# Performance work log

Measured on AMD Instinct MI355X. Metric: run time of the kernel, lower is better.

Reference implementation:

```python
import jax, jax.numpy as jnp
import numpy as np

NUM_HEADS = 8
QUERY_HEAD_DIM = 32
POS_HEAD_DIM = 4
EMBED_DIM = 512
POS_DIM = 192
SEQ_LEN = 1024
BATCH = 8
IN_PROJ_DIM = (QUERY_HEAD_DIM * 2 + POS_HEAD_DIM) * NUM_HEADS  # 544


def setup_inputs() -> dict:
    key = jax.random.key(0)
    k1, k2, k3, k4, k5 = jax.random.split(key, 5)
    x = jax.random.normal(k1, (SEQ_LEN, BATCH, EMBED_DIM), dtype=jnp.float32)
    pos_emb = jax.random.normal(k2, (1, 2 * SEQ_LEN - 1, POS_DIM), dtype=jnp.float32)
    key_padding_mask = jnp.zeros((BATCH, SEQ_LEN), dtype=bool)
    # in_proj: ScaledLinear(embed_dim -> in_proj_dim) with initial_scale qhd**-0.25
    scale_in = QUERY_HEAD_DIM ** (-0.25) / np.sqrt(EMBED_DIM)
    W_in = jax.random.normal(k3, (EMBED_DIM, IN_PROJ_DIM), dtype=jnp.float32) * scale_in
    b_in = jax.random.normal(k4, (IN_PROJ_DIM,), dtype=jnp.float32) * 0.01
    # linear_pos: ScaledLinear(pos_dim -> num_heads*pos_head_dim), no bias, scale 0.05
    W_pos = jax.random.normal(k5, (POS_DIM, NUM_HEADS * POS_HEAD_DIM), dtype=jnp.float32) * (0.05 / np.sqrt(POS_DIM))
    return {"x": x, "pos_emb": pos_emb, "W_in": W_in, "b_in": b_in,
            "W_pos": W_pos, "key_padding_mask": key_padding_mask}


def reference(x, pos_emb, W_in, b_in, W_pos, key_padding_mask):
    S, B, _ = x.shape
    H, QH, PH = NUM_HEADS, QUERY_HEAD_DIM, POS_HEAD_DIM
    qd = H * QH
    xp = x @ W_in + b_in                          # (S, B, in_proj_dim)
    q = xp[..., :qd].reshape(S, B, H, QH)
    k = xp[..., qd:2 * qd].reshape(S, B, H, QH)   # Whiten/Balancer are identity in eval
    p = xp[..., 2 * qd:].reshape(S, B, H, PH)
    # content scores: (H, B, T, Sk)
    attn_scores = jnp.einsum('tbhd,sbhd->hbts', q, k)
    # positional scores
    pe = (pos_emb @ W_pos).reshape(2 * S - 1, H, PH)          # (2S-1, H, PH)
    pos_scores = jnp.einsum('tbhd,nhd->hbtn', p, pe)          # (H, B, T, 2S-1)
    # relative shift: out[h,b,t,j] = pos_scores[h,b,t, (S-1) - t + j]
    idx = (S - 1) - jnp.arange(S)[:, None] + jnp.arange(S)[None, :]  # (S, S)
    shifted = jnp.take_along_axis(pos_scores, idx[None, None, :, :], axis=-1)
    attn_scores = attn_scores + shifted
    # key padding mask: True positions get -1000 (as in masked_fill)
    attn_scores = jnp.where(key_padding_mask[None, :, None, :], -1000.0, attn_scores)
    return jax.nn.softmax(attn_scores, axis=-1)  # (H, B, T, S)
```

## Files before the change

kernel.cpp:

```cpp
#include <hip/hip_runtime.h>

#define SEQ  1024
#define BATCH 8
#define NH   8
#define EMB  512
#define QHD  32
#define PHD  4
#define PDIM 192
#define NPROJ 544
#define NPE  2047
#define L2E  1.4426950408889634f

typedef float nf4 __attribute__((ext_vector_type(4)));
typedef short bf16x8 __attribute__((ext_vector_type(8)));
typedef float f32x4 __attribute__((ext_vector_type(4)));

__device__ __forceinline__ unsigned short f2bf_rne(float f) {
    unsigned int u = __float_as_uint(f);
    unsigned int r = (u + 0x7fffu + ((u >> 16) & 1u)) >> 16;
    return (unsigned short)r;
}
__device__ __forceinline__ float bf2f(unsigned short b) {
    return __uint_as_float(((unsigned int)b) << 16);
}
__device__ __forceinline__ void cvt8(const float4 a, const float4 b, uint4& hi, uint4& lo) {
    unsigned short h0 = f2bf_rne(a.x), h1 = f2bf_rne(a.y), h2 = f2bf_rne(a.z), h3 = f2bf_rne(a.w);
    unsigned short h4 = f2bf_rne(b.x), h5 = f2bf_rne(b.y), h6 = f2bf_rne(b.z), h7 = f2bf_rne(b.w);
    unsigned short l0 = f2bf_rne(a.x - bf2f(h0)), l1 = f2bf_rne(a.y - bf2f(h1));
    unsigned short l2 = f2bf_rne(a.z - bf2f(h2)), l3 = f2bf_rne(a.w - bf2f(h3));
    unsigned short l4 = f2bf_rne(b.x - bf2f(h4)), l5 = f2bf_rne(b.y - bf2f(h5));
    unsigned short l6 = f2bf_rne(b.z - bf2f(h6)), l7 = f2bf_rne(b.w - bf2f(h7));
    hi.x = (unsigned)h0 | ((unsigned)h1 << 16); hi.y = (unsigned)h2 | ((unsigned)h3 << 16);
    hi.z = (unsigned)h4 | ((unsigned)h5 << 16); hi.w = (unsigned)h6 | ((unsigned)h7 << 16);
    lo.x = (unsigned)l0 | ((unsigned)l1 << 16); lo.y = (unsigned)l2 | ((unsigned)l3 << 16);
    lo.z = (unsigned)l4 | ((unsigned)l5 << 16); lo.w = (unsigned)l6 | ((unsigned)l7 << 16);
}

__global__ __launch_bounds__(256) void convw_kernel(const float* __restrict__ W,
                                                    unsigned short* __restrict__ whT,
                                                    unsigned short* __restrict__ wlT) {
    __shared__ float tile[32][33];
    const int n0 = blockIdx.x * 32, k0 = blockIdx.y * 32;
    const int c = threadIdx.x & 31, r0 = threadIdx.x >> 5;
#pragma unroll
    for (int i = 0; i < 4; ++i) {
        int r = r0 + i * 8;
        tile[r][c] = W[(size_t)(k0 + r) * NPROJ + n0 + c];
    }
    __syncthreads();
#pragma unroll
    for (int i = 0; i < 4; ++i) {
        int n = r0 + i * 8;
        float v = tile[c][n];
        unsigned short h = f2bf_rne(v);
        unsigned short l = f2bf_rne(v - bf2f(h));
        whT[(size_t)(n0 + n) * 512 + k0 + c] = h;
        wlT[(size_t)(n0 + n) * 512 + k0 + c] = l;
    }
}

__global__ __launch_bounds__(128) void pe_kernel(const float* __restrict__ pos_emb,
                                                 const float* __restrict__ W_pos,
                                                 float* __restrict__ peg) {
    const int n = blockIdx.x * 128 + threadIdx.x;
    const int h = blockIdx.y;
    if (n >= NPE) return;
    const float* pr = pos_emb + (size_t)n * PDIM;
    float a0 = 0.f, a1 = 0.f, a2 = 0.f, a3 = 0.f;
    for (int c = 0; c < PDIM; c += 4) {
        float4 pv = *(const float4*)(pr + c);
#pragma unroll
        for (int cc = 0; cc < 4; ++cc) {
            float pvc = cc == 0 ? pv.x : cc == 1 ? pv.y : cc == 2 ? pv.z : pv.w;
            float4 w4 = *(const float4*)(W_pos + (c + cc) * 32 + h * 4);
            a0 += pvc * w4.x; a1 += pvc * w4.y; a2 += pvc * w4.z; a3 += pvc * w4.w;
        }
    }
    float4 o;
    o.x = a0 * L2E; o.y = a1 * L2E; o.z = a2 * L2E; o.w = a3 * L2E;
    *(float4*)(peg + ((size_t)h * NPE + n) * 4) = o;
}

__global__ __launch_bounds__(256) void inproj_kernel(const float* __restrict__ x,
                                                     const unsigned short* __restrict__ whT,
                                                     const unsigned short* __restrict__ wlT,
                                                     const float* __restrict__ bias,
                                                     unsigned short* __restrict__ qhi,
                                                     unsigned short* __restrict__ qlo,
                                                     unsigned short* __restrict__ khi,
                                                     unsigned short* __restrict__ klo,
                                                     float* __restrict__ pws) {
    __shared__ __align__(16) unsigned short xh_l[8][128][8];
    __shared__ __align__(16) unsigned short xl_l[8][128][8];
    __shared__ __align__(16) unsigned short wh_l[8][32][8];
    __shared__ __align__(16) unsigned short wl_l[8][32][8];

    const int bid = blockIdx.x;
    const int xcd = bid & 7;
    const int L   = xcd * 136 + (bid >> 3);
    const int mb  = L / 17;
    const int nb  = L - mb * 17;

    const int tid = threadIdx.x, lane = tid & 63, w = tid >> 6;
    const int la = lane & 15, lb = lane >> 4;
    const int m0 = mb * 128, n0 = nb * 32;

    const int mx = tid >> 1, k8x = (tid & 1) * 4;
    const int nw = tid >> 3, k8w = tid & 7;

    f32x4 acc[2][2];
#pragma unroll
    for (int mt = 0; mt < 2; ++mt)
#pragma unroll
        for (int nt = 0; nt < 2; ++nt) acc[mt][nt] = (f32x4){0.f, 0.f, 0.f, 0.f};

    for (int step = 0; step < 8; ++step) {
        const int k0 = step * 64;
        const float* sx = x + (size_t)(m0 + mx) * EMB + k0 + k8x * 8;
#pragma unroll
        for (int j = 0; j < 4; ++j) {
            float4 a = *(const float4*)(sx + j * 8);
            float4 b = *(const float4*)(sx + j * 8 + 4);
            uint4 hi, lo;
            cvt8(a, b, hi, lo);
            *(uint4*)&xh_l[k8x + j][mx][0] = hi;
            *(uint4*)&xl_l[k8x + j][mx][0] = lo;
        }
        *(uint4*)&wh_l[k8w][nw][0] = *(const uint4*)(whT + (size_t)(n0 + nw) * 512 + k0 + k8w * 8);
        *(uint4*)&wl_l[k8w][nw][0] = *(const uint4*)(wlT + (size_t)(n0 + nw) * 512 + k0 + k8w * 8);
        __syncthreads();
#pragma unroll
        for (int ks = 0; ks < 2; ++ks) {
            bf16x8 bh[2], bl[2], ah[2], al[2];
#pragma unroll
            for (int mt = 0; mt < 2; ++mt) {
                bh[mt] = *(const bf16x8*)&xh_l[ks * 4 + lb][w * 32 + mt * 16 + la][0];
                bl[mt] = *(const bf16x8*)&xl_l[ks * 4 + lb][w * 32 + mt * 16 + la][0];
            }
#pragma unroll
            for (int nt = 0; nt < 2; ++nt) {
                ah[nt] = *(const bf16x8*)&wh_l[ks * 4 + lb][nt * 16 + la][0];
                al[nt] = *(const bf16x8*)&wl_l[ks * 4 + lb][nt * 16 + la][0];
            }
#pragma unroll
            for (int mt = 0; mt < 2; ++mt)
#pragma unroll
                for (int nt = 0; nt < 2; ++nt) {
                    acc[mt][nt] = __builtin_amdgcn_mfma_f32_16x16x32_bf16(ah[nt], bh[mt], acc[mt][nt], 0, 0, 0);
                    acc[mt][nt] = __builtin_amdgcn_mfma_f32_16x16x32_bf16(ah[nt], bl[mt], acc[mt][nt], 0, 0, 0);
                    acc[mt][nt] = __builtin_amdgcn_mfma_f32_16x16x32_bf16(al[nt], bh[mt], acc[mt][nt], 0, 0, 0);
                }
        }
        __syncthreads();
    }

    const int by = nb;
#pragma unroll
    for (int mt = 0; mt < 2; ++mt) {
        const int m = m0 + w * 32 + mt * 16 + la;
        const int s = m >> 3, bb = m & 7;
#pragma unroll
        for (int nt = 0; nt < 2; ++nt) {
            const int dloc = nt * 16 + lb * 4;
            float4 b4 = *(const float4*)(bias + n0 + dloc);
            float v0 = acc[mt][nt][0] + b4.x;
            float v1 = acc[mt][nt][1] + b4.y;
            float v2 = acc[mt][nt][2] + b4.z;
            float v3 = acc[mt][nt][3] + b4.w;
            if (by < 16) {
                const int h = by & 7;
                size_t base = (((size_t)(h * 8 + bb) * SEQ + s) * 32 + dloc);
                if (by < 8) {
                    v0 *= L2E; v1 *= L2E; v2 *= L2E; v3 *= L2E;
                }
                ushort4 hi, lo;
                hi.x = f2bf_rne(v0); lo.x = f2bf_rne(v0 - bf2f(hi.x));
                hi.y = f2bf_rne(v1); lo.y = f2bf_rne(v1 - bf2f(hi.y));
                hi.z = f2bf_rne(v2); lo.z = f2bf_rne(v2 - bf2f(hi.z));
                hi.w = f2bf_rne(v3); lo.w = f2bf_rne(v3 - bf2f(hi.w));
                if (by < 8) {
                    *(ushort4*)(qhi + base) = hi;
                    *(ushort4*)(qlo + base) = lo;
                } else {
                    *(ushort4*)(khi + base) = hi;
                    *(ushort4*)(klo + base) = lo;
                }
            } else {
                const int h = nt * 4 + lb;
                float4 o; o.x = v0; o.y = v1; o.z = v2; o.w = v3;
                *(float4*)(pws + ((size_t)(h * 8 + bb) * SEQ + s) * 4) = o;
            }
        }
    }
}

__global__ __launch_bounds__(256, 3) void attn_kernel(const unsigned short* __restrict__ qhi,
                                                      const unsigned short* __restrict__ qlo,
                                                      const unsigned short* __restrict__ khi,
                                                      const unsigned short* __restrict__ klo,
                                                      const float* __restrict__ pws,
                                                      const float* __restrict__ peg,
                                                      const unsigned char* __restrict__ km,
                                                      float* __restrict__ out) {
    __shared__ float4 pe_lds[1040];
    __shared__ float red_s[16][4];

    const int bid = blockIdx.x;
    const int hb = bid & 63;
    const int h = hb >> 3, b = hb & 7;
    const int t0 = (bid >> 6) * 16;
    const int tid = threadIdx.x, lane = tid & 63;
    const int j_s = tid >> 6;
    const int la = lane & 15, lb = lane >> 4;

    const int nbase = (SEQ - 1) - t0 - 15;
    const float4* pegq = (const float4*)peg + (size_t)h * NPE + nbase;
#pragma unroll
    for (int it = 0; it < 5; ++it) {
        int idx = it * 256 + tid;
        if (idx < 1039) pe_lds[idx] = pegq[idx];
    }
    __syncthreads();

    const int t = t0 + la;
    const size_t qoff = ((size_t)hb * SEQ + t) * 32 + lb * 8;
    const bf16x8 bqh = *(const bf16x8*)(qhi + qoff);
    const bf16x8 bql = *(const bf16x8*)(qlo + qoff);

    const unsigned short* khb = khi + (size_t)hb * (SEQ * 32);
    const unsigned short* klb = klo + (size_t)hb * (SEQ * 32);

    f32x4 acc[16];
#pragma unroll
    for (int m = 0; m < 16; ++m) acc[m] = (f32x4){0.f, 0.f, 0.f, 0.f};

#pragma unroll
    for (int m = 0; m < 16; ++m) {
        const int srow = j_s * 256 + m * 16 + la;
        const bf16x8 ah = *(const bf16x8*)(khb + (size_t)srow * 32 + lb * 8);
        const bf16x8 al = *(const bf16x8*)(klb + (size_t)srow * 32 + lb * 8);
        acc[m] = __builtin_amdgcn_mfma_f32_16x16x32_bf16(ah, bqh, acc[m], 0, 0, 0);
        acc[m] = __builtin_amdgcn_mfma_f32_16x16x32_bf16(ah, bql, acc[m], 0, 0, 0);
        acc[m] = __builtin_amdgcn_mfma_f32_16x16x32_bf16(al, bqh, acc[m], 0, 0, 0);
    }

    const float4 pvv = *(const float4*)(pws + ((size_t)hb * SEQ + t) * 4);
    const int lane_off = j_s * 256 + lb * 4 + 15 - la;
#pragma unroll
    for (int m = 0; m < 16; ++m) {
        const int o = lane_off + m * 16;
#pragma unroll
        for (int j = 0; j < 4; ++j) {
            float4 e = pe_lds[o + j];
            acc[m][j] += pvv.x * e.x + pvv.y * e.y + pvv.z * e.z + pvv.w * e.w;
        }
    }

    const unsigned int* kmw = (const unsigned int*)(km + b * SEQ);
    unsigned int mk[16], mor = 0;
#pragma unroll
    for (int m = 0; m < 16; ++m) { mk[m] = kmw[j_s * 64 + m * 4 + lb]; mor |= mk[m]; }
    if (__any(mor != 0)) {
#pragma unroll
        for (int m = 0; m < 16; ++m) {
            if (mk[m] & 0x000000ffu) acc[m][0] = -1443.0f;
            if (mk[m] & 0x0000ff00u) acc[m][1] = -1443.0f;
            if (mk[m] & 0x00ff0000u) acc[m][2] = -1443.0f;
            if (mk[m] & 0xff000000u) acc[m][3] = -1443.0f;
        }
    }

    float sum = 0.f;
#pragma unroll
    for (int m = 0; m < 16; ++m) {
        acc[m][0] = __builtin_amdgcn_exp2f(acc[m][0]);
        acc[m][1] = __builtin_amdgcn_exp2f(acc[m][1]);
        acc[m][2] = __builtin_amdgcn_exp2f(acc[m][2]);
        acc[m][3] = __builtin_amdgcn_exp2f(acc[m][3]);
        sum += (acc[m][0] + acc[m][1]) + (acc[m][2] + acc[m][3]);
    }
    sum += __shfl_xor(sum, 16, 64);
    sum += __shfl_xor(sum, 32, 64);
    if (lane < 16) red_s[lane][j_s] = sum;
    __syncthreads();
    const float inv = 1.0f / ((red_s[la][0] + red_s[la][1]) + (red_s[la][2] + red_s[la][3]));

    float* op = out + ((size_t)hb * SEQ + t) * SEQ;
#pragma unroll
    for (int m = 0; m < 16; ++m) {
        nf4 o;
        o.x = acc[m][0] * inv;
        o.y = acc[m][1] * inv;
        o.z = acc[m][2] * inv;
        o.w = acc[m][3] * inv;
        *(nf4*)(op + j_s * 256 + m * 16 + lb * 4) = o;
    }
}

extern "C" void kernel_launch(void* const* d_in, const int* in_sizes, int n_in,
                              void* d_out, int out_size, void* d_ws, size_t ws_size,
                              hipStream_t stream) {
    const float* x       = (const float*)d_in[0];
    const float* pos_emb = (const float*)d_in[1];
    const float* W_in    = (const float*)d_in[2];
    const float* b_in    = (const float*)d_in[3];
    const float* W_pos   = (const float*)d_in[4];
    const unsigned char* km = (const unsigned char*)d_in[5];
    float* out = (float*)d_out;

    char* ws = (char*)d_ws;
    const size_t MB = 1024 * 1024;
    unsigned short* qhi = (unsigned short*)(ws);
    unsigned short* qlo = (unsigned short*)(ws + 4 * MB);
    unsigned short* khi = (unsigned short*)(ws + 8 * MB);
    unsigned short* klo = (unsigned short*)(ws + 12 * MB);
    float*          pws = (float*)(ws + 16 * MB);
    float*          peg = (float*)(ws + 17 * MB);
    unsigned short* whT = (unsigned short*)(ws + 18 * MB);
    unsigned short* wlT = (unsigned short*)(ws + 19 * MB);

    hipLaunchKernelGGL(convw_kernel, dim3(17, 16), dim3(256), 0, stream, W_in, whT, wlT);
    hipLaunchKernelGGL(pe_kernel, dim3(16, 8), dim3(128), 0, stream, pos_emb, W_pos, peg);
    hipLaunchKernelGGL(inproj_kernel, dim3(1088), dim3(256), 0, stream,
                       x, whT, wlT, b_in, qhi, qlo, khi, klo, pws);
    hipLaunchKernelGGL(attn_kernel, dim3(4096), dim3(256), 0, stream,
                       qhi, qlo, khi, klo, pws, peg, km, out);
}
```

Before: 157.9 us.

## Prefetch GEMM tiles into registers, stage softmax output via LDS for coalesced nontemporal stores

The projection GEMM now loads the next k-step of x and the weights into registers before the barrier, so global load latency overlaps the MFMA work of the current step. Intermediate q/k/p writes switch to nontemporal stores. In the attention kernel, the softmax output, which is the dominant 32 MB write, is transposed through a reused LDS buffer in four passes, so each wave writes whole contiguous rows with nontemporal stores instead of scattered 16-byte pieces. The cost is extra LDS traffic, eight more barriers per block, and higher register pressure in the GEMM.

```diff
diff --git a/kernel.cpp b/kernel.cpp
--- a/kernel.cpp
+++ b/kernel.cpp
@@ -12,6 +12,7 @@
 #define L2E  1.4426950408889634f
 
 typedef float nf4 __attribute__((ext_vector_type(4)));
+typedef unsigned short us4 __attribute__((ext_vector_type(4)));
 typedef short bf16x8 __attribute__((ext_vector_type(8)));
 typedef float f32x4 __attribute__((ext_vector_type(4)));
 
@@ -108,6 +109,18 @@
     const int mx = tid >> 1, k8x = (tid & 1) * 4;
     const int nw = tid >> 3, k8w = tid & 7;
 
+    const float* sx = x + (size_t)(m0 + mx) * EMB + k8x * 8;
+    const unsigned short* swh = whT + (size_t)(n0 + nw) * 512 + k8w * 8;
+    const unsigned short* swl = wlT + (size_t)(n0 + nw) * 512 + k8w * 8;
+    float4 xa[4], xb[4];
+#pragma unroll
+    for (int j = 0; j < 4; ++j) {
+        xa[j] = *(const float4*)(sx + j * 8);
+        xb[j] = *(const float4*)(sx + j * 8 + 4);
+    }
+    uint4 wwh = *(const uint4*)swh;
+    uint4 wwl = *(const uint4*)swl;
+
     f32x4 acc[2][2];
 #pragma unroll
     for (int mt = 0; mt < 2; ++mt)
@@ -115,19 +128,25 @@
         for (int nt = 0; nt < 2; ++nt) acc[mt][nt] = (f32x4){0.f, 0.f, 0.f, 0.f};
 
     for (int step = 0; step < 8; ++step) {
-        const int k0 = step * 64;
-        const float* sx = x + (size_t)(m0 + mx) * EMB + k0 + k8x * 8;
 #pragma unroll
         for (int j = 0; j < 4; ++j) {
-            float4 a = *(const float4*)(sx + j * 8);
-            float4 b = *(const float4*)(sx + j * 8 + 4);
             uint4 hi, lo;
-            cvt8(a, b, hi, lo);
+            cvt8(xa[j], xb[j], hi, lo);
             *(uint4*)&xh_l[k8x + j][mx][0] = hi;
             *(uint4*)&xl_l[k8x + j][mx][0] = lo;
         }
-        *(uint4*)&wh_l[k8w][nw][0] = *(const uint4*)(whT + (size_t)(n0 + nw) * 512 + k0 + k8w * 8);
-        *(uint4*)&wl_l[k8w][nw][0] = *(const uint4*)(wlT + (size_t)(n0 + nw) * 512 + k0 + k8w * 8);
+        *(uint4*)&wh_l[k8w][nw][0] = wwh;
+        *(uint4*)&wl_l[k8w][nw][0] = wwl;
+        if (step < 7) {
+            sx += 64; swh += 64; swl += 64;
+#pragma unroll
+            for (int j = 0; j < 4; ++j) {
+                xa[j] = *(const float4*)(sx + j * 8);
+                xb[j] = *(const float4*)(sx + j * 8 + 4);
+            }
+            wwh = *(const uint4*)swh;
+            wwl = *(const uint4*)swl;
+        }
         __syncthreads();
 #pragma unroll
         for (int ks = 0; ks < 2; ++ks) {
@@ -173,22 +192,23 @@
                 if (by < 8) {
                     v0 *= L2E; v1 *= L2E; v2 *= L2E; v3 *= L2E;
                 }
-                ushort4 hi, lo;
+                us4 hi, lo;
                 hi.x = f2bf_rne(v0); lo.x = f2bf_rne(v0 - bf2f(hi.x));
                 hi.y = f2bf_rne(v1); lo.y = f2bf_rne(v1 - bf2f(hi.y));
                 hi.z = f2bf_rne(v2); lo.z = f2bf_rne(v2 - bf2f(hi.z));
                 hi.w = f2bf_rne(v3); lo.w = f2bf_rne(v3 - bf2f(hi.w));
                 if (by < 8) {
-                    *(ushort4*)(qhi + base) = hi;
-                    *(ushort4*)(qlo + base) = lo;
+                    __builtin_nontemporal_store(hi, (us4*)(qhi + base));
+                    __builtin_nontemporal_store(lo, (us4*)(qlo + base));
                 } else {
-                    *(ushort4*)(khi + base) = hi;
-                    *(ushort4*)(klo + base) = lo;
+                    __builtin_nontemporal_store(hi, (us4*)(khi + base));
+                    __builtin_nontemporal_store(lo, (us4*)(klo + base));
                 }
             } else {
                 const int h = nt * 4 + lb;
-                float4 o; o.x = v0; o.y = v1; o.z = v2; o.w = v3;
-                *(float4*)(pws + ((size_t)(h * 8 + bb) * SEQ + s) * 4) = o;
+                nf4 o;
+                o.x = v0; o.y = v1; o.z = v2; o.w = v3;
+                __builtin_nontemporal_store(o, (nf4*)(pws + ((size_t)(h * 8 + bb) * SEQ + s) * 4));
             }
         }
     }
@@ -202,8 +222,10 @@
                                                       const float* __restrict__ peg,
                                                       const unsigned char* __restrict__ km,
                                                       float* __restrict__ out) {
-    __shared__ float4 pe_lds[1040];
+    __shared__ __align__(16) unsigned char smem_u[16640];
     __shared__ float red_s[16][4];
+    float4* pe_lds = (float4*)smem_u;
+    float*  xp_lds = (float*)smem_u;
 
     const int bid = blockIdx.x;
     const int hb = bid & 63;
@@ -285,15 +307,33 @@
     __syncthreads();
     const float inv = 1.0f / ((red_s[la][0] + red_s[la][1]) + (red_s[la][2] + red_s[la][3]));
 
-    float* op = out + ((size_t)hb * SEQ + t) * SEQ;
-#pragma unroll
-    for (int m = 0; m < 16; ++m) {
-        nf4 o;
-        o.x = acc[m][0] * inv;
-        o.y = acc[m][1] * inv;
-        o.z = acc[m][2] * inv;
-        o.w = acc[m][3] * inv;
-        *(nf4*)(op + j_s * 256 + m * 16 + lb * 4) = o;
+    const int rowi = tid >> 6;
+#pragma unroll
+    for (int p = 0; p < 4; ++p) {
+        if ((la >> 2) == p) {
+            const int r = la & 3;
+            float* rp = xp_lds + r * 1028 + j_s * 256 + lb * 4;
+#pragma unroll
+            for (int m = 0; m < 16; ++m) {
+                nf4 o;
+                o.x = acc[m][0] * inv;
+                o.y = acc[m][1] * inv;
+                o.z = acc[m][2] * inv;
+                o.w = acc[m][3] * inv;
+                *(nf4*)(rp + m * 16) = o;
+            }
+        }
+        __syncthreads();
+        {
+            const float* src = xp_lds + rowi * 1028;
+            float* op = out + ((size_t)hb * SEQ + t0 + p * 4 + rowi) * SEQ;
+#pragma unroll
+            for (int it = 0; it < 4; ++it) {
+                nf4 v = *(const nf4*)(src + it * 256 + lane * 4);
+                __builtin_nontemporal_store(v, (nf4*)(op + it * 256 + lane * 4));
+            }
+        }
+        __syncthreads();
     }
 }
 
```

Result: no change. 159.1 us (+0.8%).
